# Optimization experiments

Hardware: AMD Instinct MI355X
Metric: run time of the kernel (lower is better)

Reference implementation:

```python
import jax, jax.numpy as jnp
import numpy as np

MARGIN = 0.1  # init kwarg: margin
# type_of_distance='euclidean', type_of_quadruplets='hard', what_is_hard='one'


def _distance_euclidean(x):
    # l2-normalize rows, then all-pairs euclidean distance (torch.cdist p=2)
    x = x / jnp.linalg.norm(x, axis=1, keepdims=True)
    sq = jnp.sum(x * x, axis=1)
    d2 = sq[:, None] + sq[None, :] - 2.0 * (x @ x.T)
    return jnp.sqrt(jnp.maximum(d2, 0.0))


def setup_inputs() -> dict:
    key = jax.random.key(0)
    k1, k2 = jax.random.split(key)
    B, D, C = 256, 512, 80
    logits = jax.random.normal(k1, (B, D), dtype=jnp.float32)
    # sparse multi-hot labels: ~2.4 active classes per sample
    labels = (jax.random.uniform(k2, (B, C)) < 0.03).astype(jnp.float32)
    return {"logits": logits, "labels": labels}


def reference(logits, labels):
    n = labels.shape[0]
    sames = (labels @ labels.T) > 0                      # [B,B] bool
    diffs = ~sames
    sames = sames & ~jnp.eye(n, dtype=bool)              # fill_diagonal_(0)
    triu = jnp.triu(jnp.ones((n, n), dtype=bool), k=1)   # J < K
    # O(B^3) quadruplet-candidate mask: sames[I,J] & sames[I,K] & (J<K)
    mask = sames[:, :, None] & sames[:, None, :] & triu[None, :, :]
    I, J, K = jnp.nonzero(mask)                          # row-major, same as torch.where
    # expand each (I,J,K) triplet with every negative N of anchor I
    rows, cols = jnp.nonzero(diffs[I])                   # [n_quads]
    quadruplets = jnp.stack([I[rows], J[rows], K[rows], cols], axis=1)

    mat = _distance_euclidean(jax.lax.stop_gradient(logits))  # logits.detach()
    Ii, Jj, Kk, Nn = quadruplets[:, 0], quadruplets[:, 1], quadruplets[:, 2], quadruplets[:, 3]
    ij = mat[Ii, Jj]
    ik = mat[Ii, Kk]
    innd = mat[Ii, Nn]
    m1 = innd - ij
    m2 = innd - ik
    # type_of_quadruplets='hard', what_is_hard='one' (opt = OR)
    cond = ((m1 <= MARGIN) | (m2 <= MARGIN)) & ((m1 <= 0) | (m2 <= 0))
    return quadruplets[cond]
```

## Files before the change

### kernel.cpp

```cpp
#include <hip/hip_runtime.h>
#include <math.h>

#define NB 256
#define ND 512
#define NC 80
#define NSPLIT 8
#define SLOT 32640

__device__ float g_x [NB * ND];
__device__ float g_xt[ND * NB];
__device__ float g_sq[NB];
__device__ float g_ddneg[NB * NB];
__device__ unsigned long long g_m[NB * 2];
__device__ int   g_atot[NB];
__device__ int   g_abase[NB];
__device__ int   g_T[NB];
__device__ int   g_jk [NB * SLOT];
__device__ float g_thr[NB * SLOT];
__device__ int   g_cnt[NB * SLOT];

__device__ __forceinline__ int block_scan(int val, int* tmp) {
    int tid = threadIdx.x;
    __syncthreads();
    tmp[tid] = val;
    __syncthreads();
    #pragma unroll
    for (int off = 1; off < 256; off <<= 1) {
        int v = (tid >= off) ? tmp[tid - off] : 0;
        __syncthreads();
        tmp[tid] += v;
        __syncthreads();
    }
    return tmp[tid];
}

__device__ __forceinline__ int ubcount(const float* s, float thr) {
    int pos = 0;
    #pragma unroll
    for (int step = 128; step > 0; step >>= 1) {
        int np = pos + step;
        if (s[np - 1] <= thr) pos = np;
    }
    return pos;
}

__global__ __launch_bounds__(256) void k_prep(const float* __restrict__ logits,
                                              const float* __restrict__ labels) {
    int b = blockIdx.x, tid = threadIdx.x;
    __shared__ double red[NB];
    float v0 = logits[b * ND + tid];
    float v1 = logits[b * ND + 256 + tid];
    red[tid] = (double)(v0 * v0) + (double)(v1 * v1);
    __syncthreads();
    for (int off = 128; off > 0; off >>= 1) {
        if (tid < off) red[tid] += red[tid + off];
        __syncthreads();
    }
    float S = (float)red[0];
    float nrm = sqrtf(S);
    __syncthreads();
    float a0 = v0 / nrm;
    float a1 = v1 / nrm;
    g_x[b * ND + tid]          = a0;
    g_x[b * ND + 256 + tid]    = a1;
    g_xt[tid * NB + b]         = a0;
    g_xt[(tid + 256) * NB + b] = a1;
    red[tid] = (double)(a0 * a0) + (double)(a1 * a1);
    __syncthreads();
    for (int off = 128; off > 0; off >>= 1) {
        if (tid < off) red[tid] += red[tid + off];
        __syncthreads();
    }
    if (tid == 0) g_sq[b] = (float)red[0];
    int wv = tid >> 6, ln = tid & 63;
    if (wv == 0) {
        unsigned long long m0 = __ballot(labels[b * NC + ln] != 0.0f);
        if (ln == 0) g_m[2 * b] = m0;
    } else if (wv == 1) {
        bool p = (ln < 16) ? (labels[b * NC + 64 + ln] != 0.0f) : false;
        unsigned long long m1 = __ballot(p);
        if (ln == 0) g_m[2 * b + 1] = m1;
    }
}

__global__ __launch_bounds__(256) void k_count() {
    __shared__ float xi[ND];
    __shared__ float s_dd[NB], s_ddneg[NB], s_sort[NB];
    __shared__ int s_tmp[NB], s_rowbase[NB];
    __shared__ short s_plist[NB];
    int i = blockIdx.x, tid = threadIdx.x;
    xi[tid]       = g_x[i * ND + tid];
    xi[tid + 256] = g_x[i * ND + 256 + tid];
    __syncthreads();
    double dot = 0.0;
    #pragma unroll 8
    for (int c = 0; c < ND; ++c)
        dot = fma((double)xi[c], (double)g_xt[c * NB + tid], dot);
    float dotf = (float)dot;
    float sm   = g_sq[i] + g_sq[tid];
    float d2   = sm - 2.0f * dotf;
    float dv   = sqrtf(d2 > 0.0f ? d2 : 0.0f);
    s_dd[tid] = dv;
    unsigned long long mi0 = g_m[2 * i],   mi1 = g_m[2 * i + 1];
    unsigned long long mt0 = g_m[2 * tid], mt1 = g_m[2 * tid + 1];
    bool shl   = ((mi0 & mt0) | (mi1 & mt1)) != 0ULL;
    bool isPos = shl && (tid != i);
    float ddneg = shl ? INFINITY : dv;
    s_ddneg[tid] = ddneg;
    g_ddneg[i * NB + tid] = ddneg;
    int incl = block_scan(isPos ? 1 : 0, s_tmp);
    int P = s_tmp[255];
    if (isPos) s_plist[incl - 1] = (short)tid;
    if (tid < P - 1) s_rowbase[tid] = tid * (P - 1) - (tid * (tid - 1)) / 2;
    s_sort[tid] = s_ddneg[tid];
    __syncthreads();
    for (int k = 2; k <= 256; k <<= 1)
        for (int j = k >> 1; j > 0; j >>= 1) {
            int p = tid ^ j;
            float mine = s_sort[tid], oth = s_sort[p];
            bool keepmin = (((tid & k) == 0) == (tid < p));
            float res = keepmin ? fminf(mine, oth) : fmaxf(mine, oth);
            __syncthreads();
            s_sort[tid] = res;
            __syncthreads();
        }
    int T = P * (P - 1) / 2;
    if (tid == 0) g_T[i] = T;
    int total = 0;
    for (int t = tid; t < T; t += NB) {
        int a = 0;
        #pragma unroll
        for (int step = 128; step > 0; step >>= 1) {
            int na = a + step;
            if (na <= P - 2 && s_rowbase[na] <= t) a = na;
        }
        int b = a + 1 + (t - s_rowbase[a]);
        int jj = s_plist[a], kk = s_plist[b];
        float thr = fmaxf(s_dd[jj], s_dd[kk]);
        int c = ubcount(s_sort, thr);
        total += c;
        g_jk [i * SLOT + t] = jj | (kk << 8);
        g_thr[i * SLOT + t] = thr;
        g_cnt[i * SLOT + t] = c;
    }
    block_scan(total, s_tmp);
    if (tid == 0) g_atot[i] = s_tmp[255];
}

__global__ __launch_bounds__(256) void k_abase() {
    __shared__ int s_tmp[NB];
    int tid = threadIdx.x;
    int v = g_atot[tid];
    int incl = block_scan(v, s_tmp);
    g_abase[tid] = incl - v;
}

__global__ __launch_bounds__(256) void k_write(int4* __restrict__ out, int maxQuads) {
    __shared__ int s_tmp[NB], s_jk[NB], s_woff[NB];
    __shared__ float s_thr[NB];
    int i = blockIdx.x / NSPLIT;
    int split = blockIdx.x % NSPLIT;
    int tid = threadIdx.x;
    int wv = tid >> 6, ln = tid & 63;
    float vneg[4];
    #pragma unroll
    for (int r = 0; r < 4; ++r) vneg[r] = g_ddneg[i * NB + ((r << 6) | ln)];
    int T = g_T[i];
    int anchorBase = g_abase[i];
    int stripe0 = (split << 2) | wv;
    int carried = 0;
    for (int cb = 0; cb < T; cb += NB) {
        int t = cb + tid;
        int cnt = 0;
        if (t < T) {
            cnt       = g_cnt[i * SLOT + t];
            s_jk[tid] = g_jk [i * SLOT + t];
            s_thr[tid]= g_thr[i * SLOT + t];
        }
        int incl = block_scan(cnt, s_tmp);
        int chunkTotal = s_tmp[255];
        s_woff[tid] = anchorBase + carried + (incl - cnt);
        __syncthreads();
        int chunkN = (T - cb < NB) ? (T - cb) : NB;
        for (int tt = stripe0; tt < chunkN; tt += NSPLIT * 4) {
            int jk    = s_jk[tt];
            float thr = s_thr[tt];
            int base  = s_woff[tt];
            int jj = jk & 255, kk = jk >> 8;
            int cum = 0;
            #pragma unroll
            for (int r = 0; r < 4; ++r) {
                bool flag = (vneg[r] <= thr);
                unsigned long long mask = __ballot(flag);
                if (flag) {
                    int pos = base + cum + __popcll(mask & ((1ULL << ln) - 1ULL));
                    if (pos < maxQuads) out[pos] = make_int4(i, jj, kk, (r << 6) | ln);
                }
                cum += __popcll(mask);
            }
        }
        carried += chunkTotal;
        __syncthreads();
    }
}

extern "C" void kernel_launch(void* const* d_in, const int* in_sizes, int n_in,
                              void* d_out, int out_size, void* d_ws, size_t ws_size,
                              hipStream_t stream) {
    const float* logits = (const float*)d_in[0];
    const float* labels = (const float*)d_in[1];
    if (n_in >= 2 && in_sizes[0] == NB * NC && in_sizes[1] == NB * ND) {
        logits = (const float*)d_in[1];
        labels = (const float*)d_in[0];
    }
    int maxQuads = out_size / 4;

    k_prep <<<NB, NB, 0, stream>>>(logits, labels);
    k_count<<<NB, NB, 0, stream>>>();
    k_abase<<<1,  NB, 0, stream>>>();
    k_write<<<NB * NSPLIT, NB, 0, stream>>>((int4*)d_out, maxQuads);
}
```

Baseline: 196.4 us.

## Compute per-triplet write offsets in count kernel and drop abase launch

The count kernel now runs a chunked block scan over triplet counts and stores each triplet's anchor-local write offset, packed with its jk and threshold, as one int4. The write kernel redoes the small 256-element anchor-base scan itself, which removes the separate k_abase launch. Each write block also stops reloading and rescanning every chunk with block-wide barriers, so its waves can stride directly over triplets. The cost is extra barriers in the count kernel's triplet loop and a redundant 256-wide scan in each of the 2048 write blocks.

```diff
diff --git a/kernel.cpp b/kernel.cpp
--- a/kernel.cpp
+++ b/kernel.cpp
@@ -13,11 +13,8 @@
 __device__ float g_ddneg[NB * NB];
 __device__ unsigned long long g_m[NB * 2];
 __device__ int   g_atot[NB];
-__device__ int   g_abase[NB];
 __device__ int   g_T[NB];
-__device__ int   g_jk [NB * SLOT];
-__device__ float g_thr[NB * SLOT];
-__device__ int   g_cnt[NB * SLOT];
+__device__ int4  g_trip[NB * SLOT];
 
 __device__ __forceinline__ int block_scan(int val, int* tmp) {
     int tid = threadIdx.x;
@@ -126,81 +123,62 @@
         }
     int T = P * (P - 1) / 2;
     if (tid == 0) g_T[i] = T;
-    int total = 0;
-    for (int t = tid; t < T; t += NB) {
-        int a = 0;
-        #pragma unroll
-        for (int step = 128; step > 0; step >>= 1) {
-            int na = a + step;
-            if (na <= P - 2 && s_rowbase[na] <= t) a = na;
+    int carried = 0;
+    for (int cb = 0; cb < T; cb += NB) {
+        int t = cb + tid;
+        int cnt = 0, jk = 0;
+        float thr = 0.0f;
+        if (t < T) {
+            int a = 0;
+            #pragma unroll
+            for (int step = 128; step > 0; step >>= 1) {
+                int na = a + step;
+                if (na <= P - 2 && s_rowbase[na] <= t) a = na;
+            }
+            int b = a + 1 + (t - s_rowbase[a]);
+            int jj = s_plist[a], kk = s_plist[b];
+            thr = fmaxf(s_dd[jj], s_dd[kk]);
+            jk  = jj | (kk << 8);
+            cnt = ubcount(s_sort, thr);
         }
-        int b = a + 1 + (t - s_rowbase[a]);
-        int jj = s_plist[a], kk = s_plist[b];
-        float thr = fmaxf(s_dd[jj], s_dd[kk]);
-        int c = ubcount(s_sort, thr);
-        total += c;
-        g_jk [i * SLOT + t] = jj | (kk << 8);
-        g_thr[i * SLOT + t] = thr;
-        g_cnt[i * SLOT + t] = c;
+        int inc2 = block_scan(cnt, s_tmp);
+        if (t < T)
+            g_trip[i * SLOT + t] =
+                make_int4(jk, __float_as_int(thr), carried + inc2 - cnt, 0);
+        carried += s_tmp[255];
     }
-    block_scan(total, s_tmp);
-    if (tid == 0) g_atot[i] = s_tmp[255];
-}
-
-__global__ __launch_bounds__(256) void k_abase() {
-    __shared__ int s_tmp[NB];
-    int tid = threadIdx.x;
-    int v = g_atot[tid];
-    int incl = block_scan(v, s_tmp);
-    g_abase[tid] = incl - v;
+    if (tid == 0) g_atot[i] = carried;
 }
 
 __global__ __launch_bounds__(256) void k_write(int4* __restrict__ out, int maxQuads) {
-    __shared__ int s_tmp[NB], s_jk[NB], s_woff[NB];
-    __shared__ float s_thr[NB];
+    __shared__ int s_tmp[NB];
     int i = blockIdx.x / NSPLIT;
     int split = blockIdx.x % NSPLIT;
     int tid = threadIdx.x;
     int wv = tid >> 6, ln = tid & 63;
+    block_scan(g_atot[tid], s_tmp);
+    int anchorBase = s_tmp[i] - g_atot[i];
     float vneg[4];
     #pragma unroll
     for (int r = 0; r < 4; ++r) vneg[r] = g_ddneg[i * NB + ((r << 6) | ln)];
     int T = g_T[i];
-    int anchorBase = g_abase[i];
-    int stripe0 = (split << 2) | wv;
-    int carried = 0;
-    for (int cb = 0; cb < T; cb += NB) {
-        int t = cb + tid;
-        int cnt = 0;
-        if (t < T) {
-            cnt       = g_cnt[i * SLOT + t];
-            s_jk[tid] = g_jk [i * SLOT + t];
-            s_thr[tid]= g_thr[i * SLOT + t];
+    int waveId = (split << 2) | wv;
+    for (int t = waveId; t < T; t += NSPLIT * 4) {
+        int4 tr = g_trip[i * SLOT + t];
+        int jj = tr.x & 255, kk = tr.x >> 8;
+        float thr = __int_as_float(tr.y);
+        int base = anchorBase + tr.z;
+        int cum = 0;
+        #pragma unroll
+        for (int r = 0; r < 4; ++r) {
+            bool flag = (vneg[r] <= thr);
+            unsigned long long mask = __ballot(flag);
+            if (flag) {
+                int pos = base + cum + __popcll(mask & ((1ULL << ln) - 1ULL));
+                if (pos < maxQuads) out[pos] = make_int4(i, jj, kk, (r << 6) | ln);
+            }
+            cum += __popcll(mask);
         }
-        int incl = block_scan(cnt, s_tmp);
-        int chunkTotal = s_tmp[255];
-        s_woff[tid] = anchorBase + carried + (incl - cnt);
-        __syncthreads();
-        int chunkN = (T - cb < NB) ? (T - cb) : NB;
-        for (int tt = stripe0; tt < chunkN; tt += NSPLIT * 4) {
-            int jk    = s_jk[tt];
-            float thr = s_thr[tt];
-            int base  = s_woff[tt];
-            int jj = jk & 255, kk = jk >> 8;
-            int cum = 0;
-            #pragma unroll
-            for (int r = 0; r < 4; ++r) {
-                bool flag = (vneg[r] <= thr);
-                unsigned long long mask = __ballot(flag);
-                if (flag) {
-                    int pos = base + cum + __popcll(mask & ((1ULL << ln) - 1ULL));
-                    if (pos < maxQuads) out[pos] = make_int4(i, jj, kk, (r << 6) | ln);
-                }
-                cum += __popcll(mask);
-            }
-        }
-        carried += chunkTotal;
-        __syncthreads();
     }
 }
 
@@ -217,6 +195,5 @@
 
     k_prep <<<NB, NB, 0, stream>>>(logits, labels);
     k_count<<<NB, NB, 0, stream>>>();
-    k_abase<<<1,  NB, 0, stream>>>();
     k_write<<<NB * NSPLIT, NB, 0, stream>>>((int4*)d_out, maxQuads);
 }
```

Measured after the change: 196.1 us. Within noise of the previous version (-0.2%).
